# Kernel optimization log

Hardware: AMD Instinct MI355X
Metric: run time of the kernel (lower is better)

The kernel has to match this reference:

```python
import jax, jax.numpy as jnp
from jax import lax
import numpy as np

S = 4096        # sentence length (words)
L = 24          # max chars per word
VOCAB = 100000
EMB = 300       # word embedding dim
CHAR_V = 64     # char vocab
CHAR_E = 25     # char embedding dim
CH_OUT = 25     # char CNN out channels
HID = 512       # LSTM hidden per direction
T = 11          # tagset size
START, STOP = 9, 10
NEG = -10000.0


def setup_inputs() -> dict:
    key = jax.random.key(0)
    ks = jax.random.split(key, 20)
    n = lambda k, shp: (0.1 * jax.random.normal(k, shp)).astype(jnp.float32)
    transitions = n(ks[0], (T, T))
    transitions = transitions.at[START, :].set(NEG).at[:, STOP].set(NEG)
    return {
        'sentence': jax.random.randint(ks[1], (S,), 0, VOCAB),
        'chars': jax.random.randint(ks[2], (S, L), 0, CHAR_V),
        'chars2_length': jax.random.randint(ks[3], (S,), 1, L),
        'd': 0,
        'word_emb': n(ks[4], (VOCAB, EMB)),
        'char_emb': n(ks[5], (CHAR_V, CHAR_E)),
        'conv_w': n(ks[6], (CH_OUT, 1, 3, CHAR_E)),
        'conv_b': n(ks[7], (CH_OUT,)),
        'Wih_f': n(ks[8], (4 * HID, EMB + CH_OUT)),
        'Whh_f': n(ks[9], (4 * HID, HID)),
        'bih_f': n(ks[10], (4 * HID,)),
        'bhh_f': n(ks[11], (4 * HID,)),
        'Wih_b': n(ks[12], (4 * HID, EMB + CH_OUT)),
        'Whh_b': n(ks[13], (4 * HID, HID)),
        'bih_b': n(ks[14], (4 * HID,)),
        'bhh_b': n(ks[15], (4 * HID,)),
        'h2t_w': n(ks[16], (T, 2 * HID)),
        'h2t_b': n(ks[17], (T,)),
        'transitions': transitions,
    }


def _lstm_dir(x, Wih, Whh, bih, bhh, reverse):
    # x: [S, in]; returns hidden states [S, HID] (PyTorch gate order i,f,g,o)
    H = Whh.shape[1]
    def step(carry, xt):
        h, c = carry
        g = xt @ Wih.T + h @ Whh.T + bih + bhh
        i, f, gg, o = jnp.split(g, 4)
        c = jax.nn.sigmoid(f) * c + jax.nn.sigmoid(i) * jnp.tanh(gg)
        h = jax.nn.sigmoid(o) * jnp.tanh(c)
        return (h, c), h
    h0 = jnp.zeros((H,), x.dtype)
    _, hs = lax.scan(step, (h0, h0), x, reverse=reverse)
    return hs


def _get_feats(sentence, chars, word_emb, char_emb, conv_w, conv_b,
               Wih_f, Whh_f, bih_f, bhh_f, Wih_b, Whh_b, bih_b, bhh_b,
               h2t_w, h2t_b):
    # char CNN: [S,1,L,CHAR_E] -> conv(k=(3,CHAR_E), pad=(2,0)) -> [S,CH_OUT,L+2,1]
    ce = char_emb[chars][:, None, :, :]
    co = lax.conv_general_dilated(ce, conv_w, window_strides=(1, 1),
                                  padding=((2, 2), (0, 0)),
                                  dimension_numbers=('NCHW', 'OIHW', 'NCHW'))
    co = co + conv_b[None, :, None, None]
    char_feat = jnp.max(co, axis=(2, 3))              # global max-pool -> [S, CH_OUT]
    emb = jnp.concatenate([word_emb[sentence], char_feat], axis=1)  # [S, EMB+CH_OUT]
    # dropout is identity at inference
    h_f = _lstm_dir(emb, Wih_f, Whh_f, bih_f, bhh_f, reverse=False)
    h_b = _lstm_dir(emb, Wih_b, Whh_b, bih_b, bhh_b, reverse=True)
    lstm_out = jnp.concatenate([h_f, h_b], axis=1)    # [S, 2*HID]
    return lstm_out @ h2t_w.T + h2t_b                 # [S, T]


def _viterbi(feats, transitions):
    init = jnp.full((T,), NEG, feats.dtype).at[START].set(0.0)
    def step(fv, feat):
        ntv = fv[None, :] + transitions               # [T, T], [i, j]: j -> i
        bptr = jnp.argmax(ntv, axis=1)
        vit = jnp.take_along_axis(ntv, bptr[:, None], axis=1)[:, 0]
        return vit + feat, bptr
    fv, bptrs = lax.scan(step, init, feats)           # bptrs: [S, T]
    term = fv + transitions[STOP]
    term = term.at[STOP].set(NEG).at[START].set(NEG)
    best = jnp.argmax(term)
    score = term[best]
    def back(tag, bptr):
        return bptr[tag], tag
    _, path = lax.scan(back, best, bptrs, reverse=True)  # path[i] = tag at position i
    return score, path


def reference(sentence, chars, chars2_length, d, word_emb, char_emb, conv_w, conv_b,
              Wih_f, Whh_f, bih_f, bhh_f, Wih_b, Whh_b, bih_b, bhh_b,
              h2t_w, h2t_b, transitions):
    feats = _get_feats(sentence, chars, word_emb, char_emb, conv_w, conv_b,
                       Wih_f, Whh_f, bih_f, bhh_f, Wih_b, Whh_b, bih_b, bhh_b,
                       h2t_w, h2t_b)
    score, tag_seq = _viterbi(feats, transitions)
    return score, tag_seq
```

## Files before the change

### kernel.cpp

```cpp
#include <hip/hip_runtime.h>
#include <hip/hip_bf16.h>
#include <math.h>

#define SLEN 4096
#define LCH 24
#define EMB 300
#define CHE 25
#define CHO 25
#define XIN 325
#define HID 512
#define GDIM 2048
#define NTAG 11
#define TAG_START 9
#define TAG_STOP 10
#define NEGV (-10000.0f)
#define NW 32
#define SENT 0x7FC00000u

#define WT_F_O   0u
#define WT_B_O   (WT_F_O + XIN*GDIM)
#define CF_O     (WT_B_O + XIN*GDIM)
#define GF_O     (CF_O + SLEN*CHO)
#define GB_O     (GF_O + SLEN*GDIM)
#define HSF_O    (GB_O + SLEN*GDIM)
#define HSB_O    (HSF_O + SLEN*HID)
#define FEATS_O  (HSB_O + SLEN*HID)

__device__ __forceinline__ float sigm(float x) { return 1.0f / (1.0f + expf(-x)); }

__global__ void k_fill(unsigned* __restrict__ p, int n, unsigned val) {
    int i = blockIdx.x * 256 + threadIdx.x;
    int stride = gridDim.x * 256;
    for (; i < n; i += stride) p[i] = val;
}

__global__ __launch_bounds__(256) void k_transpose(const float* __restrict__ wf,
        const float* __restrict__ wb, float* __restrict__ ws) {
    __shared__ float tile[32][33];
    const int dir = blockIdx.z;
    const float* src = dir ? wb : wf;
    float* dst = ws + (dir ? WT_B_O : WT_F_O);
    const int k0 = blockIdx.x * 32, j0 = blockIdx.y * 32;
    const int tx = threadIdx.x, ty = threadIdx.y;
    for (int yy = ty; yy < 32; yy += 8) {
        int k = k0 + tx;
        tile[yy][tx] = (k < XIN) ? src[(size_t)(j0 + yy) * XIN + k] : 0.f;
    }
    __syncthreads();
    for (int yy = ty; yy < 32; yy += 8) {
        int k = k0 + yy;
        if (k < XIN) dst[(size_t)k * GDIM + j0 + tx] = tile[tx][yy];
    }
}

__global__ __launch_bounds__(64) void k_charcnn(const int* __restrict__ chars,
        const float* __restrict__ cemb, const float* __restrict__ cw,
        const float* __restrict__ cb, float* __restrict__ ws) {
    int s = blockIdx.x, tid = threadIdx.x;
    __shared__ int ch[LCH];
    __shared__ float ce[LCH][CHE];
    if (tid < LCH) ch[tid] = chars[s * LCH + tid];
    __syncthreads();
    for (int idx = tid; idx < LCH * CHE; idx += 64) {
        int l = idx / CHE, e = idx % CHE;
        ce[l][e] = cemb[ch[l] * CHE + e];
    }
    __syncthreads();
    if (tid < CHO) {
        float best = -1e30f;
        for (int h = 0; h < LCH + 2; ++h) {
            float acc = cb[tid];
            #pragma unroll
            for (int kh = 0; kh < 3; ++kh) {
                int l = h - 2 + kh;
                if (l >= 0 && l < LCH) {
                    const float* wp = cw + tid * 75 + kh * CHE;
                    #pragma unroll
                    for (int e = 0; e < CHE; ++e) acc += ce[l][e] * wp[e];
                }
            }
            best = fmaxf(best, acc);
        }
        (ws + CF_O)[s * CHO + tid] = best;
    }
}

__global__ __launch_bounds__(256) void k_ingemm(const int* __restrict__ sent,
        const float* __restrict__ wemb,
        const float* __restrict__ bih_f, const float* __restrict__ bhh_f,
        const float* __restrict__ bih_b, const float* __restrict__ bhh_b,
        float* __restrict__ ws) {
    const int rt = blockIdx.x, jt = blockIdx.y, dir = blockIdx.z;
    const float* wt = ws + (dir ? WT_B_O : WT_F_O);
    const float* cf = ws + CF_O;
    float* g = ws + (dir ? GB_O : GF_O);
    const float* bih = dir ? bih_b : bih_f;
    const float* bhh = dir ? bhh_b : bhh_f;
    __shared__ float xt[XIN][32];
    __shared__ int sl[32];
    const int tid = threadIdx.x;
    const int r0 = rt * 32, j0 = jt * 256;
    if (tid < 32) sl[tid] = sent[r0 + tid];
    __syncthreads();
    for (int idx = tid; idx < XIN * 32; idx += 256) {
        int k = idx >> 5, r = idx & 31;
        float v = (k < EMB) ? wemb[(size_t)sl[r] * EMB + k]
                            : cf[(size_t)(r0 + r) * CHO + (k - EMB)];
        xt[k][r] = v;
    }
    __syncthreads();
    const int jg = tid & 31, rg = tid >> 5;
    const int jb = j0 + jg * 8, rb = rg * 4;
    float acc[4][8];
    #pragma unroll
    for (int a = 0; a < 4; ++a)
        #pragma unroll
        for (int b = 0; b < 8; ++b) acc[a][b] = 0.f;
    for (int k = 0; k < XIN; ++k) {
        float4 xv = *(const float4*)&xt[k][rb];
        const float4* wp = (const float4*)(wt + (size_t)k * GDIM + jb);
        float4 w0 = wp[0], w1 = wp[1];
        float xr[4] = {xv.x, xv.y, xv.z, xv.w};
        float wv[8] = {w0.x, w0.y, w0.z, w0.w, w1.x, w1.y, w1.z, w1.w};
        #pragma unroll
        for (int a = 0; a < 4; ++a)
            #pragma unroll
            for (int b = 0; b < 8; ++b) acc[a][b] += xr[a] * wv[b];
    }
    float bs[8];
    #pragma unroll
    for (int b = 0; b < 8; ++b) bs[b] = bih[jb + b] + bhh[jb + b];
    #pragma unroll
    for (int a = 0; a < 4; ++a) {
        float* gp = g + (size_t)(r0 + rb + a) * GDIM + jb;
        #pragma unroll
        for (int b = 0; b < 8; ++b) gp[b] = acc[a][b] + bs[b];
    }
}

__global__ __launch_bounds__(256, 1) void k_lstm(const float* __restrict__ whh_f,
        const float* __restrict__ whh_b, float* __restrict__ ws) {
    const int wg = blockIdx.x;
    const int dir = wg >> 5;
    const int w = wg & 31;
    const int tid = threadIdx.x;
    const int wave = tid >> 6;
    const int lane = tid & 63;
    const int hbase = w * 16;
    const int q = lane >> 4, hj = lane & 15;
    const int grow = q * HID + hbase + hj;
    const float* whh = dir ? whh_b : whh_f;
    const float* gin_p = ws + (dir ? GB_O : GF_O);
    float* hs = ws + (dir ? HSB_O : HSF_O);

    float4 W[32];
    const float4* wsrc = (const float4*)(whh + (size_t)grow * HID + wave * 128);
    #pragma unroll
    for (int i = 0; i < 32; ++i) W[i] = wsrc[i];

    __shared__ __align__(16) float h_lds[HID];
    __shared__ float part_lds[256];
    for (int i = tid; i < HID; i += 256) h_lds[i] = 0.f;
    float c = 0.f;
    __syncthreads();

    int s = dir ? (SLEN - 1) : 0;
    float gin = 0.f;
    if (tid < 64) gin = gin_p[(size_t)s * GDIM + grow];

    for (int t = 0; t < SLEN; ++t) {
        float4 a = {0.f, 0.f, 0.f, 0.f};
        const float4* h4 = (const float4*)(h_lds + wave * 128);
        #pragma unroll
        for (int i = 0; i < 32; ++i) {
            float4 h = h4[i];
            a.x += W[i].x * h.x; a.y += W[i].y * h.y;
            a.z += W[i].z * h.z; a.w += W[i].w * h.w;
        }
        part_lds[tid] = (a.x + a.y) + (a.z + a.w);
        __syncthreads();

        if (tid < 64) {
            float gsum = part_lds[lane] + part_lds[64 + lane]
                       + part_lds[128 + lane] + part_lds[192 + lane] + gin;
            float gi = __shfl(gsum, hj);
            float gf = __shfl(gsum, 16 + hj);
            float gg = __shfl(gsum, 32 + hj);
            float go = __shfl(gsum, 48 + hj);
            if (lane < 16) {
                c = sigm(gf) * c + sigm(gi) * tanhf(gg);
                float h = sigm(go) * tanhf(c);
                __hip_atomic_store((unsigned*)&hs[(size_t)s * HID + hbase + lane],
                                   __float_as_uint(h),
                                   __ATOMIC_RELAXED, __HIP_MEMORY_SCOPE_AGENT);
            }
        }

        const int sn = dir ? (s - 1) : (s + 1);
        const int sc = (t + 1 < SLEN) ? sn : s;
        if (tid < 64) gin = gin_p[(size_t)sc * GDIM + grow];

        const unsigned long long* srcp =
            (const unsigned long long*)(hs + (size_t)s * HID) + tid;
        unsigned long long v;
        do {
            v = __hip_atomic_load(srcp, __ATOMIC_RELAXED, __HIP_MEMORY_SCOPE_AGENT);
        } while ((unsigned)v == SENT || (unsigned)(v >> 32) == SENT);
        ((unsigned long long*)h_lds)[tid] = v;
        __syncthreads();
        s = sc;
    }
}

__global__ __launch_bounds__(64) void k_feats(const float* __restrict__ h2tw,
        const float* __restrict__ h2tb, float* __restrict__ ws) {
    const int s = blockIdx.x, l = threadIdx.x;
    const float* hf = ws + HSF_O + (size_t)s * HID;
    const float* hb = ws + HSB_O + (size_t)s * HID;
    float xf[8], xb[8];
    #pragma unroll
    for (int m = 0; m < 8; ++m) { xf[m] = hf[l + 64 * m]; xb[m] = hb[l + 64 * m]; }
    float* feats = ws + FEATS_O;
    for (int t = 0; t < NTAG; ++t) {
        const float* wp = h2tw + (size_t)t * (2 * HID);
        float p = 0.f;
        #pragma unroll
        for (int m = 0; m < 8; ++m)
            p += xf[m] * wp[l + 64 * m] + xb[m] * wp[HID + l + 64 * m];
        #pragma unroll
        for (int o = 32; o; o >>= 1) p += __shfl_down(p, o);
        if (l == 0) feats[(size_t)s * NTAG + t] = p + h2tb[t];
    }
}

__global__ __launch_bounds__(64) void k_viterbi(const float* __restrict__ trans,
        float* __restrict__ ws, float* __restrict__ out) {
    const int lane = threadIdx.x;
    __shared__ float fbuf[256 * NTAG];
    __shared__ unsigned char bp[SLEN * NTAG];
    const float* feats = ws + FEATS_O;
    const int li = (lane < NTAG) ? lane : 0;
    float trow[NTAG];
    #pragma unroll
    for (int jj = 0; jj < NTAG; ++jj)
        trow[jj] = (lane < NTAG) ? trans[lane * NTAG + jj] : NEGV;
    float fv = (lane == TAG_START) ? 0.f : NEGV;
    for (int ch = 0; ch < SLEN / 256; ++ch) {
        for (int idx = lane; idx < 256 * NTAG; idx += 64)
            fbuf[idx] = feats[(size_t)ch * 256 * NTAG + idx];
        __syncthreads();
        for (int ss = 0; ss < 256; ++ss) {
            const int s = ch * 256 + ss;
            float best = -1e30f; int bj = 0;
            #pragma unroll
            for (int jj = 0; jj < NTAG; ++jj) {
                float v = __shfl(fv, jj) + trow[jj];
                if (v > best) { best = v; bj = jj; }
            }
            fv = best + fbuf[ss * NTAG + li];
            if (lane < NTAG) bp[s * NTAG + lane] = (unsigned char)bj;
        }
        __syncthreads();
    }
    float term = fv + ((lane < NTAG) ? trans[TAG_STOP * NTAG + lane] : NEGV);
    if (lane == TAG_START || lane == TAG_STOP) term = NEGV;
    float bestv = -1e30f; int bt = 0;
    #pragma unroll
    for (int jj = 0; jj < NTAG; ++jj) {
        float v = __shfl(term, jj);
        if (v > bestv) { bestv = v; bt = jj; }
    }
    unsigned char* path = (unsigned char*)fbuf;
    if (lane == 0) {
        int tag = bt;
        for (int s2 = SLEN - 1; s2 >= 0; --s2) {
            path[s2] = (unsigned char)tag;
            tag = bp[s2 * NTAG + tag];
        }
        out[0] = bestv;
    }
    __syncthreads();
    for (int idx = lane; idx < SLEN; idx += 64)
        out[1 + idx] = (float)path[idx];
}

extern "C" void kernel_launch(void* const* d_in, const int* in_sizes, int n_in,
                              void* d_out, int out_size, void* d_ws, size_t ws_size,
                              hipStream_t stream) {
    const int*   sentence = (const int*)  d_in[0];
    const int*   chars    = (const int*)  d_in[1];
    const float* word_emb = (const float*)d_in[4];
    const float* char_emb = (const float*)d_in[5];
    const float* conv_w   = (const float*)d_in[6];
    const float* conv_b   = (const float*)d_in[7];
    const float* Wih_f    = (const float*)d_in[8];
    const float* Whh_f    = (const float*)d_in[9];
    const float* bih_f    = (const float*)d_in[10];
    const float* bhh_f    = (const float*)d_in[11];
    const float* Wih_b    = (const float*)d_in[12];
    const float* Whh_b    = (const float*)d_in[13];
    const float* bih_b    = (const float*)d_in[14];
    const float* bhh_b    = (const float*)d_in[15];
    const float* h2t_w    = (const float*)d_in[16];
    const float* h2t_b    = (const float*)d_in[17];
    const float* trans    = (const float*)d_in[18];
    float* ws  = (float*)d_ws;
    float* out = (float*)d_out;

    k_fill<<<2048, 256, 0, stream>>>((unsigned*)(ws + HSF_O), 2 * SLEN * HID, SENT);
    k_transpose<<<dim3((XIN + 31) / 32, GDIM / 32, 2), dim3(32, 8), 0, stream>>>(
        Wih_f, Wih_b, ws);
    k_charcnn<<<SLEN, 64, 0, stream>>>(chars, char_emb, conv_w, conv_b, ws);
    k_ingemm<<<dim3(SLEN / 32, GDIM / 256, 2), 256, 0, stream>>>(
        sentence, word_emb, bih_f, bhh_f, bih_b, bhh_b, ws);
    k_lstm<<<2 * NW, 256, 0, stream>>>(Whh_f, Whh_b, ws);
    k_feats<<<SLEN, 64, 0, stream>>>(h2t_w, h2t_b, ws);
    k_viterbi<<<1, 64, 0, stream>>>(trans, ws, out);
}
```

Baseline: 10.56 ms.

## Fuse forward and backward LSTM recurrences into one workgroup per hidden slice

The LSTM recurrence kernel now runs both directions in the same workgroup. It holds both Whh slices in registers and polls the forward and backward hidden rows in a single spin loop, with half as many workgroups. Each thread interleaves two independent dot products, and the two cross-workgroup waits overlap instead of running in separate blocks. In exchange, per-thread register use for weights doubles, which risks spills or AGPR use, and each step does twice the work on fewer CUs.

```diff
diff --git a/kernel.cpp b/kernel.cpp
--- a/kernel.cpp
+++ b/kernel.cpp
@@ -140,49 +140,58 @@
 
 __global__ __launch_bounds__(256, 1) void k_lstm(const float* __restrict__ whh_f,
         const float* __restrict__ whh_b, float* __restrict__ ws) {
-    const int wg = blockIdx.x;
-    const int dir = wg >> 5;
-    const int w = wg & 31;
+    const int w = blockIdx.x;
     const int tid = threadIdx.x;
     const int wave = tid >> 6;
     const int lane = tid & 63;
     const int hbase = w * 16;
     const int q = lane >> 4, hj = lane & 15;
     const int grow = q * HID + hbase + hj;
-    const float* whh = dir ? whh_b : whh_f;
-    const float* gin_p = ws + (dir ? GB_O : GF_O);
-    float* hs = ws + (dir ? HSB_O : HSF_O);
-
-    float4 W[32];
-    const float4* wsrc = (const float4*)(whh + (size_t)grow * HID + wave * 128);
-    #pragma unroll
-    for (int i = 0; i < 32; ++i) W[i] = wsrc[i];
-
-    __shared__ __align__(16) float h_lds[HID];
-    __shared__ float part_lds[256];
-    for (int i = tid; i < HID; i += 256) h_lds[i] = 0.f;
+    const float* gf_p = ws + GF_O;
+    const float* gb_p = ws + GB_O;
+    float* hsf = ws + HSF_O;
+    float* hsb = ws + HSB_O;
+
+    float4 Wf[32], Wb[32];
+    {
+        const float4* s0 = (const float4*)(whh_f + (size_t)grow * HID + wave * 128);
+        const float4* s1 = (const float4*)(whh_b + (size_t)grow * HID + wave * 128);
+        #pragma unroll
+        for (int i = 0; i < 32; ++i) { Wf[i] = s0[i]; Wb[i] = s1[i]; }
+    }
+
+    __shared__ __align__(16) float hf_lds[HID];
+    __shared__ __align__(16) float hb_lds[HID];
+    __shared__ float pf[256], pb[256];
+    for (int i = tid; i < HID; i += 256) { hf_lds[i] = 0.f; hb_lds[i] = 0.f; }
     float c = 0.f;
     __syncthreads();
 
-    int s = dir ? (SLEN - 1) : 0;
+    int sf = 0, sb = SLEN - 1;
     float gin = 0.f;
-    if (tid < 64) gin = gin_p[(size_t)s * GDIM + grow];
+    if (tid < 64)       gin = gf_p[(size_t)sf * GDIM + grow];
+    else if (tid < 128) gin = gb_p[(size_t)sb * GDIM + grow];
 
     for (int t = 0; t < SLEN; ++t) {
-        float4 a = {0.f, 0.f, 0.f, 0.f};
-        const float4* h4 = (const float4*)(h_lds + wave * 128);
+        float4 af = {0.f, 0.f, 0.f, 0.f}, ab = {0.f, 0.f, 0.f, 0.f};
+        const float4* h4f = (const float4*)(hf_lds + wave * 128);
+        const float4* h4b = (const float4*)(hb_lds + wave * 128);
         #pragma unroll
         for (int i = 0; i < 32; ++i) {
-            float4 h = h4[i];
-            a.x += W[i].x * h.x; a.y += W[i].y * h.y;
-            a.z += W[i].z * h.z; a.w += W[i].w * h.w;
-        }
-        part_lds[tid] = (a.x + a.y) + (a.z + a.w);
+            float4 hf = h4f[i], hb = h4b[i];
+            af.x += Wf[i].x * hf.x; af.y += Wf[i].y * hf.y;
+            af.z += Wf[i].z * hf.z; af.w += Wf[i].w * hf.w;
+            ab.x += Wb[i].x * hb.x; ab.y += Wb[i].y * hb.y;
+            ab.z += Wb[i].z * hb.z; ab.w += Wb[i].w * hb.w;
+        }
+        pf[tid] = (af.x + af.y) + (af.z + af.w);
+        pb[tid] = (ab.x + ab.y) + (ab.z + ab.w);
         __syncthreads();
 
-        if (tid < 64) {
-            float gsum = part_lds[lane] + part_lds[64 + lane]
-                       + part_lds[128 + lane] + part_lds[192 + lane] + gin;
+        if (tid < 128) {
+            const float* part = (tid < 64) ? pf : pb;
+            float gsum = part[lane] + part[64 + lane]
+                       + part[128 + lane] + part[192 + lane] + gin;
             float gi = __shfl(gsum, hj);
             float gf = __shfl(gsum, 16 + hj);
             float gg = __shfl(gsum, 32 + hj);
@@ -190,25 +199,41 @@
             if (lane < 16) {
                 c = sigm(gf) * c + sigm(gi) * tanhf(gg);
                 float h = sigm(go) * tanhf(c);
-                __hip_atomic_store((unsigned*)&hs[(size_t)s * HID + hbase + lane],
+                float* row = (tid < 64) ? (hsf + (size_t)sf * HID)
+                                        : (hsb + (size_t)sb * HID);
+                __hip_atomic_store((unsigned*)&row[hbase + lane],
                                    __float_as_uint(h),
                                    __ATOMIC_RELAXED, __HIP_MEMORY_SCOPE_AGENT);
             }
         }
 
-        const int sn = dir ? (s - 1) : (s + 1);
-        const int sc = (t + 1 < SLEN) ? sn : s;
-        if (tid < 64) gin = gin_p[(size_t)sc * GDIM + grow];
-
-        const unsigned long long* srcp =
-            (const unsigned long long*)(hs + (size_t)s * HID) + tid;
-        unsigned long long v;
+        const int sfn = (t + 1 < SLEN) ? sf + 1 : sf;
+        const int sbn = (t + 1 < SLEN) ? sb - 1 : sb;
+        if (tid < 64)       gin = gf_p[(size_t)sfn * GDIM + grow];
+        else if (tid < 128) gin = gb_p[(size_t)sbn * GDIM + grow];
+
+        const unsigned long long* pfp =
+            (const unsigned long long*)(hsf + (size_t)sf * HID) + tid;
+        const unsigned long long* pbp =
+            (const unsigned long long*)(hsb + (size_t)sb * HID) + tid;
+        unsigned long long vf = 0, vb = 0;
+        bool okf = false, okb = false;
         do {
-            v = __hip_atomic_load(srcp, __ATOMIC_RELAXED, __HIP_MEMORY_SCOPE_AGENT);
-        } while ((unsigned)v == SENT || (unsigned)(v >> 32) == SENT);
-        ((unsigned long long*)h_lds)[tid] = v;
+            if (!okf) {
+                vf = __hip_atomic_load(pfp, __ATOMIC_RELAXED,
+                                       __HIP_MEMORY_SCOPE_AGENT);
+                okf = ((unsigned)vf != SENT) && ((unsigned)(vf >> 32) != SENT);
+            }
+            if (!okb) {
+                vb = __hip_atomic_load(pbp, __ATOMIC_RELAXED,
+                                       __HIP_MEMORY_SCOPE_AGENT);
+                okb = ((unsigned)vb != SENT) && ((unsigned)(vb >> 32) != SENT);
+            }
+        } while (!(okf && okb));
+        ((unsigned long long*)hf_lds)[tid] = vf;
+        ((unsigned long long*)hb_lds)[tid] = vb;
         __syncthreads();
-        s = sc;
+        sf = sfn; sb = sbn;
     }
 }
 
@@ -313,7 +338,7 @@
     k_charcnn<<<SLEN, 64, 0, stream>>>(chars, char_emb, conv_w, conv_b, ws);
     k_ingemm<<<dim3(SLEN / 32, GDIM / 256, 2), 256, 0, stream>>>(
         sentence, word_emb, bih_f, bhh_f, bih_b, bhh_b, ws);
-    k_lstm<<<2 * NW, 256, 0, stream>>>(Whh_f, Whh_b, ws);
+    k_lstm<<<NW, 256, 0, stream>>>(Whh_f, Whh_b, ws);
     k_feats<<<SLEN, 64, 0, stream>>>(h2t_w, h2t_b, ws);
     k_viterbi<<<1, 64, 0, stream>>>(trans, ws, out);
 }
```

Measured after the change: 22.27 ms. 111% more time.

## Pin LSTM directions to single XCDs, drop barrier, use fast activations

Applied to the files above, without the earlier changes.

The recurrent LSTM kernel launches 256 blocks and keeps only the ones on XCDs 0 and 1, so each direction's 32 cooperating blocks share one L2 for their per-step hidden-state exchange. This relies on round-robin block-to-XCD dispatch. The partial-sum LDS buffer is double-buffered and the trailing __syncthreads is removed, since each wave only reads the h slice its own lanes wrote. Gate activations switch to __expf plus hardware reciprocal, which trades a little accuracy for a shorter serial step.

```diff
diff --git a/kernel.cpp b/kernel.cpp
--- a/kernel.cpp
+++ b/kernel.cpp
@@ -27,6 +27,13 @@
 #define FEATS_O  (HSB_O + SLEN*HID)
 
 __device__ __forceinline__ float sigm(float x) { return 1.0f / (1.0f + expf(-x)); }
+
+__device__ __forceinline__ float frcp(float x) { return __builtin_amdgcn_rcpf(x); }
+__device__ __forceinline__ float fsigm(float x) { return frcp(1.0f + __expf(-x)); }
+__device__ __forceinline__ float ftanh(float x) {
+    float e = __expf(2.0f * x);
+    return 1.0f - 2.0f * frcp(e + 1.0f);
+}
 
 __global__ void k_fill(unsigned* __restrict__ p, int n, unsigned val) {
     int i = blockIdx.x * 256 + threadIdx.x;
@@ -140,9 +147,14 @@
 
 __global__ __launch_bounds__(256, 1) void k_lstm(const float* __restrict__ whh_f,
         const float* __restrict__ whh_b, float* __restrict__ ws) {
-    const int wg = blockIdx.x;
-    const int dir = wg >> 5;
-    const int w = wg & 31;
+    const int xcd = blockIdx.x & 7;
+    const int idx = blockIdx.x >> 3;
+    if (idx >= NW) return;
+    int dir;
+    if (xcd == 0) dir = 0;
+    else if (xcd == 1) dir = 1;
+    else return;
+    const int w = idx;
     const int tid = threadIdx.x;
     const int wave = tid >> 6;
     const int lane = tid & 63;
@@ -159,7 +171,7 @@
     for (int i = 0; i < 32; ++i) W[i] = wsrc[i];
 
     __shared__ __align__(16) float h_lds[HID];
-    __shared__ float part_lds[256];
+    __shared__ float part_lds[2][256];
     for (int i = tid; i < HID; i += 256) h_lds[i] = 0.f;
     float c = 0.f;
     __syncthreads();
@@ -169,6 +181,7 @@
     if (tid < 64) gin = gin_p[(size_t)s * GDIM + grow];
 
     for (int t = 0; t < SLEN; ++t) {
+        const int buf = t & 1;
         float4 a = {0.f, 0.f, 0.f, 0.f};
         const float4* h4 = (const float4*)(h_lds + wave * 128);
         #pragma unroll
@@ -177,19 +190,20 @@
             a.x += W[i].x * h.x; a.y += W[i].y * h.y;
             a.z += W[i].z * h.z; a.w += W[i].w * h.w;
         }
-        part_lds[tid] = (a.x + a.y) + (a.z + a.w);
+        part_lds[buf][tid] = (a.x + a.y) + (a.z + a.w);
         __syncthreads();
 
         if (tid < 64) {
-            float gsum = part_lds[lane] + part_lds[64 + lane]
-                       + part_lds[128 + lane] + part_lds[192 + lane] + gin;
+            float gsum = part_lds[buf][lane] + part_lds[buf][64 + lane]
+                       + part_lds[buf][128 + lane] + part_lds[buf][192 + lane]
+                       + gin;
             float gi = __shfl(gsum, hj);
             float gf = __shfl(gsum, 16 + hj);
             float gg = __shfl(gsum, 32 + hj);
             float go = __shfl(gsum, 48 + hj);
             if (lane < 16) {
-                c = sigm(gf) * c + sigm(gi) * tanhf(gg);
-                float h = sigm(go) * tanhf(c);
+                c = fsigm(gf) * c + fsigm(gi) * ftanh(gg);
+                float h = fsigm(go) * ftanh(c);
                 __hip_atomic_store((unsigned*)&hs[(size_t)s * HID + hbase + lane],
                                    __float_as_uint(h),
                                    __ATOMIC_RELAXED, __HIP_MEMORY_SCOPE_AGENT);
@@ -207,7 +221,6 @@
             v = __hip_atomic_load(srcp, __ATOMIC_RELAXED, __HIP_MEMORY_SCOPE_AGENT);
         } while ((unsigned)v == SENT || (unsigned)(v >> 32) == SENT);
         ((unsigned long long*)h_lds)[tid] = v;
-        __syncthreads();
         s = sc;
     }
 }
@@ -313,7 +326,7 @@
     k_charcnn<<<SLEN, 64, 0, stream>>>(chars, char_emb, conv_w, conv_b, ws);
     k_ingemm<<<dim3(SLEN / 32, GDIM / 256, 2), 256, 0, stream>>>(
         sentence, word_emb, bih_f, bhh_f, bih_b, bhh_b, ws);
-    k_lstm<<<2 * NW, 256, 0, stream>>>(Whh_f, Whh_b, ws);
+    k_lstm<<<NW * 8, 256, 0, stream>>>(Whh_f, Whh_b, ws);
     k_feats<<<SLEN, 64, 0, stream>>>(h2t_w, h2t_b, ws);
     k_viterbi<<<1, 64, 0, stream>>>(trans, ws, out);
 }
```

After: 8.455 ms. 19.9% less time.
